# Performance work log

Hardware: AMD Instinct MI355X
Metric: run time of the kernel (lower is better)

Reference implementation:

```python
import jax, jax.numpy as jnp
import numpy as np

# TT factorization for fc1: 768 = 4*4*6*8 -> 3072 = 4*6*8*16, ranks (1,12,24,12,1)
# TT factorization for fc2: 3072 = 4*6*8*16 -> 768 = 4*4*6*8, ranks (1,12,24,12,1)
IN_F1, OUT_F1 = (4, 4, 6, 8), (4, 6, 8, 16)
IN_F2, OUT_F2 = (4, 6, 8, 16), (4, 4, 6, 8)
RANKS = (12, 24, 12)


def _core(key, shape, fan_in):
    return jax.random.normal(key, shape, dtype=jnp.float32) * (fan_in ** -0.5)


def make_tt_params(key, in_f, out_f, ranks):
    r = (1,) + tuple(ranks) + (1,)
    ks = jax.random.split(key, 5)
    # boundary cores squeeze the unit rank dims
    g1 = _core(ks[0], (in_f[0], out_f[0], r[1]), in_f[0])              # (i1,o1,r1)
    g2 = _core(ks[1], (r[1], in_f[1], out_f[1], r[2]), r[1] * in_f[1])  # (r1,i2,o2,r2)
    g3 = _core(ks[2], (r[2], in_f[2], out_f[2], r[3]), r[2] * in_f[2])  # (r2,i3,o3,r3)
    g4 = _core(ks[3], (r[3], in_f[3], out_f[3]), r[3] * in_f[3])        # (r3,i4,o4)
    b = jnp.zeros((int(np.prod(out_f)),), dtype=jnp.float32)
    return g1, g2, g3, g4, b


def tt_linear(x2d, g1, g2, g3, g4, bias, in_f):
    # x2d: (N, prod(in_f)) -> (N, prod(out_f))
    z = x2d.reshape((-1,) + tuple(in_f))                  # (b,i1,i2,i3,i4)
    z = jnp.einsum('bijkl,ipr->bjklpr', z, g1)            # (b,i2,i3,i4,o1,r1)
    z = jnp.einsum('bjklpr,rjqs->bklpqs', z, g2)          # (b,i3,i4,o1,o2,r2)
    z = jnp.einsum('bklpqs,sktu->blpqtu', z, g3)          # (b,i4,o1,o2,o3,r3)
    z = jnp.einsum('blpqtu,ulv->bpqtv', z, g4)            # (b,o1,o2,o3,o4)
    return z.reshape(z.shape[0], -1) + bias


def setup_inputs() -> dict:
    key = jax.random.key(0)
    kx, k1, k2 = jax.random.split(key, 3)
    x = jax.random.normal(kx, (2, 2048, 768), dtype=jnp.float32)
    g1a, g1b, g1c, g1d, b1 = make_tt_params(k1, IN_F1, OUT_F1, RANKS)
    g2a, g2b, g2c, g2d, b2 = make_tt_params(k2, IN_F2, OUT_F2, RANKS)
    return {"x": x, "g1a": g1a, "g1b": g1b, "g1c": g1c, "g1d": g1d, "b1": b1,
            "g2a": g2a, "g2b": g2b, "g2c": g2c, "g2d": g2d, "b2": b2}


def reference(x, g1a, g1b, g1c, g1d, b1, g2a, g2b, g2c, g2d, b2):
    B, S, D = x.shape
    h = tt_linear(x.reshape(-1, D), g1a, g1b, g1c, g1d, b1, IN_F1)  # (N, 3072)
    h = jax.nn.gelu(h, approximate=False)  # nn.GELU() default = exact erf
    # dropout: identity in eval mode
    y = tt_linear(h, g2a, g2b, g2c, g2d, b2, IN_F2)                 # (N, 768)
    return y.reshape(B, S, -1)
```

## Files before the change

kernel.cpp:

```cpp
#include <hip/hip_runtime.h>
#include <cstdint>
#include <cstddef>

typedef unsigned short u16;
typedef __attribute__((ext_vector_type(8))) __bf16 bf16x8;
typedef __attribute__((ext_vector_type(4))) float f32x4;

__device__ __forceinline__ u16 f2bf(float f) {
  unsigned u = __float_as_uint(f);
  u += 0x7FFFu + ((u >> 16) & 1u);
  return (u16)(u >> 16);
}

__device__ __forceinline__ float bf2f(u16 h) {
  return __uint_as_float(((unsigned)h) << 16);
}

__device__ __forceinline__ void async16(u16* lds, const u16* g) {
  __builtin_amdgcn_global_load_lds(
      (const __attribute__((address_space(1))) unsigned int*)g,
      (__attribute__((address_space(3))) unsigned int*)lds, 16, 0, 0);
}

__global__ __launch_bounds__(256)
void prep(const float4* __restrict__ x4, ushort4* __restrict__ xb4,
          const float* __restrict__ gA1, const float* __restrict__ gB1,
          const float* __restrict__ gC1, const float* __restrict__ gD1,
          const float* __restrict__ gA2, const float* __restrict__ gB2,
          const float* __restrict__ gC2, const float* __restrict__ gD2,
          float* __restrict__ B12_1, float* __restrict__ B12_2,
          float* __restrict__ C1, float* __restrict__ C2) {
  const int b = blockIdx.x;
  const int tid = threadIdx.x;
  if (b < 3072) {
    int i = b * 256 + tid;
    float4 v = x4[i];
    ushort4 o;
    o.x = f2bf(v.x); o.y = f2bf(v.y); o.z = f2bf(v.z); o.w = f2bf(v.w);
    xb4[i] = o;
    return;
  }
  int idx = (b - 3072) * 256 + tid;
  if (idx < 9216) {
    int e = idx;
    int r2 = e % 24; int t = e / 24;
    int fo12 = t % 24, fi12 = t / 24;
    int i2 = fi12 % 4, i1 = fi12 / 4;
    int o2 = fo12 % 6, o1 = fo12 / 6;
    float s = 0.f;
#pragma unroll
    for (int r1 = 0; r1 < 12; ++r1)
      s += gA1[(i1 * 4 + o1) * 12 + r1] * gB1[((r1 * 4 + i2) * 6 + o2) * 24 + r2];
    B12_1[e] = s;
  } else if (idx < 18432) {
    int e = idx - 9216;
    int r2 = e % 24; int t = e / 24;
    int fo12 = t % 16, fi12 = t / 16;
    int i2 = fi12 % 6, i1 = fi12 / 6;
    int o2 = fo12 % 4, o1 = fo12 / 4;
    float s = 0.f;
#pragma unroll
    for (int r1 = 0; r1 < 12; ++r1)
      s += gA2[(i1 * 4 + o1) * 12 + r1] * gB2[((r1 * 6 + i2) * 4 + o2) * 24 + r2];
    B12_2[e] = s;
  } else if (idx < 165888) {
    int e = idx - 18432;
    int fi34 = e % 48; int t = e / 48;
    int fo34 = t % 128;
    int i3 = fi34 / 8, i4 = fi34 % 8;
    int o3 = fo34 / 16, o4 = fo34 % 16;
    int r2 = t / 128;
    float s = 0.f;
#pragma unroll
    for (int r3 = 0; r3 < 12; ++r3)
      s += gC1[((r2 * 6 + i3) * 8 + o3) * 12 + r3] * gD1[(r3 * 8 + i4) * 16 + o4];
    C1[e] = s;
  } else {
    int e = idx - 165888;
    int fi34 = e % 128; int t = e / 128;
    int fo34 = t % 48;
    int i3 = fi34 / 16, i4 = fi34 % 16;
    int o3 = fo34 / 8, o4 = fo34 % 8;
    int r2 = t / 48;
    float s = 0.f;
#pragma unroll
    for (int r3 = 0; r3 < 12; ++r3)
      s += gC2[((r2 * 8 + i3) * 6 + o3) * 12 + r3] * gD2[(r3 * 16 + i4) * 8 + o4];
    C2[e] = s;
  }
}

template <int FI12, int I34, int O12, int O34, int OG>
__global__ __launch_bounds__(256)
void tt_expand(const float* __restrict__ B12, const float* __restrict__ C34t,
               u16* __restrict__ Wt) {
  constexpr int R2 = 24;
  constexpr int Kin = FI12 * I34;
  constexpr int IC = Kin / 8;
  constexpr int I34C = I34 / 8;
  __shared__ float sB[FI12 * OG * 25];
  const int tid = threadIdx.x;
  const int by = blockIdx.y;
  for (int e = tid; e < FI12 * OG * R2; e += 256) {
    int r2 = e % R2; int t = e / R2;
    int f = t % OG; int fi12 = t / OG;
    sB[(fi12 * OG + f) * 25 + r2] = B12[(fi12 * O12 + by * OG + f) * R2 + r2];
  }
  __syncthreads();
  const int t = blockIdx.x * 256 + tid;
  const int fo34 = t / IC;
  const int ic = t % IC;
  const int fi12 = ic / I34C;
  const int fi34 = (ic % I34C) * 8;

  float acc[OG][8];
#pragma unroll
  for (int f = 0; f < OG; ++f)
#pragma unroll
    for (int k = 0; k < 8; ++k) acc[f][k] = 0.f;

  for (int r2 = 0; r2 < R2; ++r2) {
    const float4* cp = (const float4*)(C34t + ((size_t)(r2 * O34 + fo34) * I34 + fi34));
    float4 c0 = cp[0], c1 = cp[1];
    float c[8] = {c0.x, c0.y, c0.z, c0.w, c1.x, c1.y, c1.z, c1.w};
#pragma unroll
    for (int f = 0; f < OG; ++f) {
      float bb = sB[(fi12 * OG + f) * 25 + r2];
#pragma unroll
      for (int k = 0; k < 8; ++k) acc[f][k] += bb * c[k];
    }
  }
#pragma unroll
  for (int f = 0; f < OG; ++f) {
    int out = (by * OG + f) * O34 + fo34;
    u16 v[8];
#pragma unroll
    for (int k = 0; k < 8; ++k) v[k] = f2bf(acc[f][k]);
    *(uint4*)(Wt + (size_t)out * Kin + fi12 * I34 + fi34) = *(const uint4*)v;
  }
}

__global__ void reduceN8(const uint4* __restrict__ P, const float* __restrict__ bias,
                         float4* __restrict__ out4, int n8, int zstride8, int nz) {
  int i = blockIdx.x * 256 + threadIdx.x;
  if (i >= n8) return;
  int b0 = (i % 96) * 8;
  float a[8];
#pragma unroll
  for (int k = 0; k < 8; ++k) a[k] = bias[b0 + k];
  for (int s = 0; s < nz; ++s) {
    uint4 u = P[i + s * zstride8];
    const u16* up = (const u16*)&u;
#pragma unroll
    for (int k = 0; k < 8; ++k) a[k] += bf2f(up[k]);
  }
  out4[i * 2]     = (float4){a[0], a[1], a[2], a[3]};
  out4[i * 2 + 1] = (float4){a[4], a[5], a[6], a[7]};
}

template <bool GELU>
__global__ __launch_bounds__(256, 3)
void gemm_bt(const u16* __restrict__ A, const u16* __restrict__ Bt,
             const float* __restrict__ bias, u16* __restrict__ Out,
             int N, int K, int klen, size_t zstride) {
  __shared__ __align__(16) u16 As[2][128 * 32];
  __shared__ __align__(16) u16 Bs[2][128 * 32];
  const int tid = threadIdx.x;
  const int bm = blockIdx.x, bn = blockIdx.y;
  const int wave = tid >> 6, lane = tid & 63;
  const int wm = (wave & 1) * 64, wn = (wave >> 1) * 64;
  const int lr = lane & 15, lq = lane >> 4;

  const int srow = tid >> 2;
  const int scol = (tid & 3) * 8;
  const u16* Ag = A + (size_t)(bm * 128 + srow) * K + scol;
  const u16* Bg = Bt + (size_t)(bn * 128 + srow) * K + scol;
  u16* AsW = &As[0][0] + tid * 8;
  u16* BsW = &Bs[0][0] + tid * 8;

  f32x4 acc[4][4];
#pragma unroll
  for (int i = 0; i < 4; i++)
#pragma unroll
    for (int j = 0; j < 4; j++) acc[i][j] = (f32x4){0.f, 0.f, 0.f, 0.f};

  const int kbeg = blockIdx.z * klen;
  const int nIter = klen >> 5;

  auto stage = [&](int buf, int k0) {
    async16(AsW + buf * 4096,        Ag + k0);
    async16(AsW + buf * 4096 + 2048, Ag + k0 + (size_t)64 * K);
    async16(BsW + buf * 4096,        Bg + k0);
    async16(BsW + buf * 4096 + 2048, Bg + k0 + (size_t)64 * K);
  };
  auto compute = [&](int buf) {
    bf16x8 af[4], bfr[4];
#pragma unroll
    for (int i = 0; i < 4; i++)
      af[i] = *(const bf16x8*)(&As[buf][0] + (wm + i * 16 + lr) * 32 + lq * 8);
#pragma unroll
    for (int j = 0; j < 4; j++)
      bfr[j] = *(const bf16x8*)(&Bs[buf][0] + (wn + j * 16 + lr) * 32 + lq * 8);
#pragma unroll
    for (int i = 0; i < 4; i++)
#pragma unroll
      for (int j = 0; j < 4; j++)
        acc[i][j] = __builtin_amdgcn_mfma_f32_16x16x32_bf16(af[i], bfr[j], acc[i][j], 0, 0, 0);
  };

  stage(0, kbeg);
  for (int it = 0; it < nIter; it += 2) {
    __syncthreads();
    if (it + 1 < nIter) stage(1, kbeg + (it + 1) * 32);
    compute(0);
    __syncthreads();
    if (it + 2 < nIter) stage(0, kbeg + (it + 2) * 32);
    compute(1);
  }

  u16* Op = Out + blockIdx.z * zstride;
  const int r0 = bm * 128 + wm + lq * 4;
  const int c0 = bn * 128 + wn + lr;
  float bv[4];
  if (GELU) {
#pragma unroll
    for (int j = 0; j < 4; j++) bv[j] = bias[c0 + j * 16];
  }
#pragma unroll
  for (int i = 0; i < 4; i++) {
#pragma unroll
    for (int r = 0; r < 4; r++) {
      const size_t rowoff = (size_t)(r0 + i * 16 + r) * N;
#pragma unroll
      for (int j = 0; j < 4; j++) {
        float v = acc[i][j][r];
        if (GELU) {
          v += bv[j];
          v = 0.5f * v * (1.f + erff(v * 0.70710678118654752f));
        }
        Op[rowoff + c0 + j * 16] = f2bf(v);
      }
    }
  }
}

extern "C" void kernel_launch(void* const* d_in, const int* in_sizes, int n_in,
                              void* d_out, int out_size, void* d_ws, size_t ws_size,
                              hipStream_t stream) {
  const float* x   = (const float*)d_in[0];
  const float* g1a = (const float*)d_in[1];
  const float* g1b = (const float*)d_in[2];
  const float* g1c = (const float*)d_in[3];
  const float* g1d = (const float*)d_in[4];
  const float* b1  = (const float*)d_in[5];
  const float* g2a = (const float*)d_in[6];
  const float* g2b = (const float*)d_in[7];
  const float* g2c = (const float*)d_in[8];
  const float* g2d = (const float*)d_in[9];
  const float* b2  = (const float*)d_in[10];
  float* out = (float*)d_out;

  char* ws = (char*)d_ws;
  u16* xb   = (u16*)(ws + 0);
  u16* W1t  = (u16*)(ws + 6291456);
  u16* W2t  = (u16*)(ws + 11010048);
  u16* h    = (u16*)(ws + 15728640);
  u16* Part = (u16*)(ws + 40894464);
  float* B12_1 = (float*)(ws + 40894464);
  float* B12_2 = (float*)(ws + 40894464 + 36864);
  float* C1    = (float*)(ws + 40894464 + 73728);
  float* C2    = (float*)(ws + 40894464 + 663552);

  prep<<<4296, 256, 0, stream>>>((const float4*)x, (ushort4*)xb,
                                 g1a, g1b, g1c, g1d, g2a, g2b, g2c, g2d,
                                 B12_1, B12_2, C1, C2);

  tt_expand<16, 48, 24, 128, 4><<<dim3(48, 6), 256, 0, stream>>>(B12_1, C1, W1t);
  tt_expand<24, 128, 16, 48, 4><<<dim3(72, 4), 256, 0, stream>>>(B12_2, C2, W2t);

  gemm_bt<true><<<dim3(32, 24, 1), 256, 0, stream>>>(xb, W1t, b1, h, 3072, 768, 768, 0);
  gemm_bt<false><<<dim3(32, 6, 4), 256, 0, stream>>>(h, W2t, nullptr, Part,
                                                     768, 3072, 768, 3145728);
  reduceN8<<<1536, 256, 0, stream>>>((const uint4*)Part, b2,
                                     (float4*)out, 393216, 393216, 4);
}
```

Baseline: 181.2 us.

## Merge TT expand launches and raise split-K factor for second GEMM

Fuses the two tt_expand launches into a single kernel that dispatches on block index, removing one launch. The second GEMM's split-K factor goes from 4 to 8 when the workspace is large enough, giving more blocks (6x32x8) to fill the GPU. Its launch-bounds occupancy hint rises to 4. The cost is more bf16 partial-sum traffic and extra reduction work in reduceN8, plus possible register pressure from the tighter launch bound.

```diff
diff --git a/kernel.cpp b/kernel.cpp
--- a/kernel.cpp
+++ b/kernel.cpp
@@ -91,23 +91,20 @@
 }
 
 template <int FI12, int I34, int O12, int O34, int OG>
-__global__ __launch_bounds__(256)
-void tt_expand(const float* __restrict__ B12, const float* __restrict__ C34t,
-               u16* __restrict__ Wt) {
+__device__ __forceinline__
+void tt_expand_body(const float* __restrict__ B12, const float* __restrict__ C34t,
+                    u16* __restrict__ Wt, int bx, int by, int tid, float* sB) {
   constexpr int R2 = 24;
   constexpr int Kin = FI12 * I34;
   constexpr int IC = Kin / 8;
   constexpr int I34C = I34 / 8;
-  __shared__ float sB[FI12 * OG * 25];
-  const int tid = threadIdx.x;
-  const int by = blockIdx.y;
   for (int e = tid; e < FI12 * OG * R2; e += 256) {
     int r2 = e % R2; int t = e / R2;
     int f = t % OG; int fi12 = t / OG;
     sB[(fi12 * OG + f) * 25 + r2] = B12[(fi12 * O12 + by * OG + f) * R2 + r2];
   }
   __syncthreads();
-  const int t = blockIdx.x * 256 + tid;
+  const int t = bx * 256 + tid;
   const int fo34 = t / IC;
   const int ic = t % IC;
   const int fi12 = ic / I34C;
@@ -137,6 +134,20 @@
 #pragma unroll
     for (int k = 0; k < 8; ++k) v[k] = f2bf(acc[f][k]);
     *(uint4*)(Wt + (size_t)out * Kin + fi12 * I34 + fi34) = *(const uint4*)v;
+  }
+}
+
+__global__ __launch_bounds__(256)
+void tt_expand2(const float* __restrict__ B12_1, const float* __restrict__ C1, u16* __restrict__ W1t,
+                const float* __restrict__ B12_2, const float* __restrict__ C2, u16* __restrict__ W2t) {
+  __shared__ float sB[24 * 4 * 25];
+  const int b = blockIdx.x;
+  const int tid = threadIdx.x;
+  if (b < 288) {
+    tt_expand_body<16, 48, 24, 128, 4>(B12_1, C1, W1t, b % 48, b / 48, tid, sB);
+  } else {
+    int bb = b - 288;
+    tt_expand_body<24, 128, 16, 48, 4>(B12_2, C2, W2t, bb % 72, bb / 72, tid, sB);
   }
 }
 
@@ -158,8 +169,8 @@
   out4[i * 2 + 1] = (float4){a[4], a[5], a[6], a[7]};
 }
 
-template <bool GELU>
-__global__ __launch_bounds__(256, 3)
+template <bool GELU, int MINW>
+__global__ __launch_bounds__(256, MINW)
 void gemm_bt(const u16* __restrict__ A, const u16* __restrict__ Bt,
              const float* __restrict__ bias, u16* __restrict__ Out,
              int N, int K, int klen, size_t zstride) {
@@ -271,16 +282,17 @@
   float* C1    = (float*)(ws + 40894464 + 73728);
   float* C2    = (float*)(ws + 40894464 + 663552);
 
+  const int nz = (ws_size >= 40894464ull + 8ull * 6291456ull) ? 8 : 4;
+
   prep<<<4296, 256, 0, stream>>>((const float4*)x, (ushort4*)xb,
                                  g1a, g1b, g1c, g1d, g2a, g2b, g2c, g2d,
                                  B12_1, B12_2, C1, C2);
 
-  tt_expand<16, 48, 24, 128, 4><<<dim3(48, 6), 256, 0, stream>>>(B12_1, C1, W1t);
-  tt_expand<24, 128, 16, 48, 4><<<dim3(72, 4), 256, 0, stream>>>(B12_2, C2, W2t);
-
-  gemm_bt<true><<<dim3(32, 24, 1), 256, 0, stream>>>(xb, W1t, b1, h, 3072, 768, 768, 0);
-  gemm_bt<false><<<dim3(32, 6, 4), 256, 0, stream>>>(h, W2t, nullptr, Part,
-                                                     768, 3072, 768, 3145728);
+  tt_expand2<<<576, 256, 0, stream>>>(B12_1, C1, W1t, B12_2, C2, W2t);
+
+  gemm_bt<true, 3><<<dim3(32, 24, 1), 256, 0, stream>>>(xb, W1t, b1, h, 3072, 768, 768, 0);
+  gemm_bt<false, 4><<<dim3(32, 6, nz), 256, 0, stream>>>(h, W2t, nullptr, Part,
+                                                         768, 3072, 3072 / nz, 3145728);
   reduceN8<<<1536, 256, 0, stream>>>((const uint4*)Part, b2,
-                                     (float4*)out, 393216, 393216, 4);
-}
+                                     (float4*)out, 393216, 393216, nz);
+}
```

Result: faster. 176.4 us (-2.7%).
